# Performance work log

Hardware: AMD Instinct MI355X
Metric: run time of the kernel (lower is better)

The kernel has to match this reference:

```python
import jax, jax.numpy as jnp
import numpy as np

WS = 7            # cubic window
HEADS = 6
DIM = 96          # attention channel dim (concat of two half-streams)
CH = 48           # per-stream channels (dim // 2)
HID = 384         # int(dim * mlp_ratio)
N = WS ** 3       # 343 tokens per window
EPS = 1e-5


def _rel_pos_index():
    c = np.stack(np.meshgrid(np.arange(WS), np.arange(WS), np.arange(WS), indexing='ij')).reshape(3, -1)
    rel = (c[:, :, None] - c[:, None, :]).transpose(1, 2, 0) + (WS - 1)
    rel[:, :, 0] *= (2 * WS - 1) * (2 * WS - 1)
    rel[:, :, 1] *= (2 * WS - 1)
    return rel.sum(-1)  # (N, N) int

RPI = jnp.asarray(_rel_pos_index())


def _ln(x, g, b):
    m = x.mean(-1, keepdims=True)
    v = ((x - m) ** 2).mean(-1, keepdims=True)
    return (x - m) * jax.lax.rsqrt(v + EPS) * g + b


def _win_part(x):
    B, H, W, T, C = x.shape
    x = x.reshape(B, H // WS, WS, W // WS, WS, T // WS, WS, C)
    return x.transpose(0, 1, 3, 5, 2, 4, 6, 7).reshape(-1, WS, WS, WS, C)


def _win_rev(w, B, H, W, T):
    C = w.shape[-1]
    x = w.reshape(B, H // WS, W // WS, T // WS, WS, WS, WS, C)
    return x.transpose(0, 1, 4, 2, 5, 3, 6, 7).reshape(B, H, W, T, C)


def _chessboard(wa, wb, gd, gh, gw):
    C = wa.shape[-1]
    a = wa.reshape(gd, gh, gw, WS, WS, WS, C)
    b = wb.reshape(gd, gh, gw, WS, WS, WS, C)
    i = jnp.arange(gd)[:, None, None]
    j = jnp.arange(gh)[None, :, None]
    k = jnp.arange(gw)[None, None, :]
    m = (((i + j + k) % 2) == 0)[..., None, None, None, None]
    return (jnp.where(m, a, b).reshape(-1, WS, WS, WS, C),
            jnp.where(m, b, a).reshape(-1, WS, WS, WS, C))


def _attn(x, mask, rpb, qkv_w, qkv_b, proj_w, proj_b):
    B_, n, C = x.shape
    hd = C // HEADS
    qkv = (x @ qkv_w + qkv_b).reshape(B_, n, 3, HEADS, hd).transpose(2, 0, 3, 1, 4)
    q, k, v = qkv[0] * (hd ** -0.5), qkv[1], qkv[2]
    att = jnp.einsum('bhnd,bhmd->bhnm', q, k)
    att = att + rpb[RPI].transpose(2, 0, 1)[None]   # relative position bias gather
    att = att + mask[:, None]                        # shift mask; B_ == nW since B == 1
    att = jax.nn.softmax(att, axis=-1)
    out = jnp.einsum('bhnm,bhmd->bhnd', att, v).transpose(0, 2, 1, 3).reshape(B_, n, C)
    return out @ proj_w + proj_b


def _mlp(x, w1, b1, w2, b2):
    return jax.nn.gelu(x @ w1 + b1, approximate=False) @ w2 + b2


def _forward(x_a, x_b, mask_matrix, n1a_g, n1a_b, n1b_g, n1b_b,
             rpb_a, qkvw_a, qkvb_a, projw_a, projb_a,
             rpb_b, qkvw_b, qkvb_b, projw_b, projb_b,
             n2a_g, n2a_b, n2b_g, n2b_b,
             fc1w_a, fc1b_a, fc2w_a, fc2b_a, fc1w_b, fc1b_b, fc2w_b, fc2b_b,
             gw1, gw2, gb2, H, W, T):
    B, L, _ = x_a.shape
    sa0, sb0 = x_a, x_b
    a = _ln(x_a, n1a_g, n1a_b).reshape(B, H, W, T, CH)
    b = _ln(x_b, n1b_g, n1b_b).reshape(B, H, W, T, CH)
    # chessboard cross-stream shuffle of windows (shifted-window branch)
    ca, cb = _chessboard(_win_part(a), _win_part(b), H // WS, W // WS, T // WS)
    a_cr = _win_rev(ca, B, H, W, T)
    b_cr = _win_rev(cb, B, H, W, T)
    neg, pos, dims = (-3, -3, -3), (3, 3, 3), (1, 2, 3)
    sa, sb = jnp.roll(a, neg, dims), jnp.roll(b, neg, dims)
    sac, sbc = jnp.roll(a_cr, neg, dims), jnp.roll(b_cr, neg, dims)
    xa_w = _win_part(jnp.concatenate([sa, sbc], -1)).reshape(-1, N, DIM)
    xb_w = _win_part(jnp.concatenate([sb, sac], -1)).reshape(-1, N, DIM)
    oa = _attn(xa_w, mask_matrix, rpb_a, qkvw_a, qkvb_a, projw_a, projb_a)
    ob = _attn(xb_w, mask_matrix, rpb_b, qkvw_b, qkvb_b, projw_b, projb_b)
    oa = jnp.roll(_win_rev(oa.reshape(-1, WS, WS, WS, DIM), B, H, W, T), pos, dims)[..., :CH].reshape(B, L, CH)
    ob = jnp.roll(_win_rev(ob.reshape(-1, WS, WS, WS, DIM), B, H, W, T), pos, dims)[..., :CH].reshape(B, L, CH)
    x_a = sa0 + oa
    x_b = sb0 + ob
    x_a = x_a + _mlp(_ln(x_a, n2a_g, n2a_b), fc1w_a, fc1b_a, fc2w_a, fc2b_a)
    x_b = x_b + _mlp(_ln(x_b, n2b_g, n2b_b), fc1w_b, fc1b_b, fc2w_b, fc2b_b)
    g = jax.nn.sigmoid(jnp.maximum(x_a.mean(1) @ gw1, 0.0) @ gw2 + gb2)[:, :, None]  # (B,1,1)
    x_a = x_a + g * x_b
    return x_a, x_b


def setup_inputs():
    key = jax.random.key(0)
    ks = iter(jax.random.split(key, 24))
    H = W = T = 35
    L = H * W * T
    nW = (H // WS) * (W // WS) * (T // WS)
    p = lambda shape: jax.random.normal(next(ks), shape, jnp.float32) * 0.02
    d = {
        'x_a': jax.random.normal(next(ks), (1, L, CH), jnp.float32),
        'x_b': jax.random.normal(next(ks), (1, L, CH), jnp.float32),
        'mask_matrix': jax.random.normal(next(ks), (nW, N, N), jnp.float32),
        'n1a_g': jnp.ones((CH,), jnp.float32), 'n1a_b': jnp.zeros((CH,), jnp.float32),
        'n1b_g': jnp.ones((CH,), jnp.float32), 'n1b_b': jnp.zeros((CH,), jnp.float32),
        'rpb_a': p(((2 * WS - 1) ** 3, HEADS)),
        'qkvw_a': p((DIM, 3 * DIM)), 'qkvb_a': jnp.zeros((3 * DIM,), jnp.float32),
        'projw_a': p((DIM, DIM)), 'projb_a': jnp.zeros((DIM,), jnp.float32),
        'rpb_b': p(((2 * WS - 1) ** 3, HEADS)),
        'qkvw_b': p((DIM, 3 * DIM)), 'qkvb_b': jnp.zeros((3 * DIM,), jnp.float32),
        'projw_b': p((DIM, DIM)), 'projb_b': jnp.zeros((DIM,), jnp.float32),
        'n2a_g': jnp.ones((CH,), jnp.float32), 'n2a_b': jnp.zeros((CH,), jnp.float32),
        'n2b_g': jnp.ones((CH,), jnp.float32), 'n2b_b': jnp.zeros((CH,), jnp.float32),
        'fc1w_a': p((CH, HID)), 'fc1b_a': jnp.zeros((HID,), jnp.float32),
        'fc2w_a': p((HID, CH)), 'fc2b_a': jnp.zeros((CH,), jnp.float32),
        'fc1w_b': p((CH, HID)), 'fc1b_b': jnp.zeros((HID,), jnp.float32),
        'fc2w_b': p((HID, CH)), 'fc2b_b': jnp.zeros((CH,), jnp.float32),
        'gw1': p((CH, CH // 4)), 'gw2': p((CH // 4, 1)),
        'gb2': jnp.full((1,), -2.0, jnp.float32),
        'H': H, 'W': W, 'T': T,
    }
    return d


def reference(x_a, x_b, mask_matrix, n1a_g, n1a_b, n1b_g, n1b_b,
              rpb_a, qkvw_a, qkvb_a, projw_a, projb_a,
              rpb_b, qkvw_b, qkvb_b, projw_b, projb_b,
              n2a_g, n2a_b, n2b_g, n2b_b,
              fc1w_a, fc1b_a, fc2w_a, fc2b_a, fc1w_b, fc1b_b, fc2w_b, fc2b_b,
              gw1, gw2, gb2, H, W, T):
    return _forward(x_a, x_b, mask_matrix, n1a_g, n1a_b, n1b_g, n1b_b,
                    rpb_a, qkvw_a, qkvb_a, projw_a, projb_a,
                    rpb_b, qkvw_b, qkvb_b, projw_b, projb_b,
                    n2a_g, n2a_b, n2b_g, n2b_b,
                    fc1w_a, fc1b_a, fc2w_a, fc2b_a, fc1w_b, fc1b_b, fc2w_b, fc2b_b,
                    gw1, gw2, gb2, H, W, T)
```

## Files before the change

kernel.cpp:

```cpp
#include <hip/hip_runtime.h>
#include <hip/hip_fp16.h>

#define LQ    42875
#define NTOK  343
#define X1SZ  2058000

#define OFF_MEAN 0
#define OFF_QKV  36928
#define OFF_WF   12500000
#define OFF_RPB  12600000
#define OFF_MASKH 13400000
#define MASKH_ELEMS 14706125ull
#define QKV_BYTES_NEEDED 56100000ull
#define MASKH_BYTES_NEEDED 83100000ull

typedef _Float16 f16x8 __attribute__((ext_vector_type(8)));
typedef float f32x4 __attribute__((ext_vector_type(4)));
union B128 { uint4 u; f16x8 h; _Float16 e[8]; };

__device__ __forceinline__ int src_index(int w, int i, int& par) {
  int gi = w / 25, gj = (w / 5) % 5, gk = w % 5;
  int ph = i / 49, pw = (i / 7) % 7, pt = i % 7;
  int hs = gi * 7 + ph + 3; if (hs >= 35) hs -= 35;
  int wd = gj * 7 + pw + 3; if (wd >= 35) wd -= 35;
  int td = gk * 7 + pt + 3; if (td >= 35) td -= 35;
  par = ((hs / 7) + (wd / 7) + (td / 7)) & 1;
  return (hs * 35 + wd) * 35 + td;
}

__global__ __launch_bounds__(64) void k_init(float* __restrict__ ws) {
  if (threadIdx.x < 49) ws[threadIdx.x] = 0.f;
}

__global__ __launch_bounds__(256) void k_pack(
    const float* __restrict__ w1a, const float* __restrict__ w1b,
    const float* __restrict__ w2a, const float* __restrict__ w2b,
    const float* __restrict__ qwa, const float* __restrict__ qwb,
    float* __restrict__ ws) {
  int idx = blockIdx.x * 256 + threadIdx.x;
  if (idx >= 17664) return;
  uint4* WFB = (uint4*)(ws + OFF_WF);
  unsigned short h[8];
  uint4* dst;
  if (idx < 10752) {
    int s = idx / 5376, r = idx - s * 5376;
    uint4* WF = WFB + (size_t)s * 5376;
    if (r < 3072) {
      int jn = r / 128, t = r - jn * 128, kk = t / 64, lane = t - kk * 64;
      int q = lane >> 4, n = lane & 15;
      const float* w1 = s ? w1b : w1a;
      int j = jn * 16 + n;
#pragma unroll
      for (int e = 0; e < 8; e++) {
        int k = kk * 32 + q * 8 + e;
        float v = (k < 48) ? w1[k * 384 + j] : 0.f;
        h[e] = __half_as_ushort(__float2half(v));
      }
    } else {
      int rr = r - 3072;
      int kt = rr / 192, t = rr - kt * 192, cn = t / 64, lane = t - cn * 64;
      int q = lane >> 4, n = lane & 15;
      const float* w2 = s ? w2b : w2a;
      int c = cn * 16 + n;
#pragma unroll
      for (int e = 0; e < 8; e++) {
        int j = kt * 32 + q * 8 + e;
        h[e] = __half_as_ushort(__float2half(w2[j * 48 + c]));
      }
    }
    dst = WF + r;
  } else {
    int idx2 = idx - 10752;
    int s = idx2 / 3456, r = idx2 - s * 3456;
    int jn = r / 192, t = r - jn * 192, kk = t / 64, lane = t - kk * 64;
    int q = lane >> 4, n = lane & 15;
    const float* qw = s ? qwb : qwa;
    int j = jn * 16 + n;
#pragma unroll
    for (int e = 0; e < 8; e++) {
      int k = kk * 32 + q * 8 + e;
      h[e] = __half_as_ushort(__float2half(qw[k * 288 + j]));
    }
    dst = WFB + 10752 + (size_t)s * 3456 + r;
  }
  uint4 u;
  u.x = (unsigned)h[0] | ((unsigned)h[1] << 16);
  u.y = (unsigned)h[2] | ((unsigned)h[3] << 16);
  u.z = (unsigned)h[4] | ((unsigned)h[5] << 16);
  u.w = (unsigned)h[6] | ((unsigned)h[7] << 16);
  *dst = u;
}

__global__ __launch_bounds__(256) void k_rpb(
    const float* __restrict__ rpa, const float* __restrict__ rpbp,
    float* __restrict__ ws) {
  int sh = blockIdx.y;
  int s = sh / 6, h = sh - s * 6;
  int idx = blockIdx.x * 256 + threadIdx.x;
  if (idx >= 117649) return;
  int ir = idx / 343, j = idx - ir * 343;
  int bi = (ir / 49) * 169 + ((ir / 7) % 7) * 13 + (ir % 7) + 1098;
  int bj = (j / 49) * 169 + ((j / 7) % 7) * 13 + (j % 7);
  const float* rp = s ? rpbp : rpa;
  ((__half*)(ws + OFF_RPB))[(size_t)sh * 117649 + idx] =
      __float2half(rp[(bi - bj) * 6 + h]);
}

__global__ __launch_bounds__(256) void k_maskh(
    const float* __restrict__ mask, __half* __restrict__ mh) {
  size_t i = ((size_t)blockIdx.x * 256 + threadIdx.x) * 4;
  if (i + 4 <= MASKH_ELEMS) {
    float4 v = *(const float4*)(mask + i);
    __half2* d = (__half2*)(mh + i);
    d[0] = __floats2half2_rn(v.x, v.y);
    d[1] = __floats2half2_rn(v.z, v.w);
  } else {
    for (; i < MASKH_ELEMS; i++) mh[i] = __float2half(mask[i]);
  }
}

__global__ __launch_bounds__(256) void k_qkv(
    const float* __restrict__ xa, const float* __restrict__ xb,
    const float* __restrict__ ga, const float* __restrict__ ba,
    const float* __restrict__ gb, const float* __restrict__ bb,
    const float* __restrict__ qba, const float* __restrict__ qbb,
    const float* __restrict__ ws, __half* __restrict__ qkvh) {
  __shared__ uint4 LDSB[2368];
  int s = blockIdx.z;
  int tid = threadIdx.x;
  int wid = tid >> 6, lane = tid & 63;
  int quad = lane >> 4, n15 = lane & 15;
  uint4* WR = LDSB + wid * 592;
  _Float16* th = (_Float16*)WR;
  int tbase = blockIdx.x * 64 + wid * 16;

  if (lane < 32) {
    int tt = lane & 15, which = lane >> 4;
    int t = tbase + tt;
    float v[48];
    bool wr = false, dup = false;
    if (t < LQ) {
      int w = t / 343, i = t - w * 343;
      int par; int src = src_index(w, i, par);
      const float* xr; const float* G; const float* B;
      bool doit;
      if (which == 0) { xr = (s ? xb : xa) + src * 48; G = s ? gb : ga; B = s ? bb : ba; doit = true; dup = (par == 1); }
      else            { xr = (s ? xa : xb) + src * 48; G = s ? ga : gb; B = s ? ba : bb; doit = (par == 0); }
      if (doit) {
        float sm = 0.f, sq = 0.f;
#pragma unroll
        for (int q4 = 0; q4 < 12; q4++) {
          float4 tv = ((const float4*)xr)[q4];
          v[4 * q4] = tv.x; v[4 * q4 + 1] = tv.y; v[4 * q4 + 2] = tv.z; v[4 * q4 + 3] = tv.w;
          sm += tv.x + tv.y + tv.z + tv.w;
          sq += tv.x * tv.x + tv.y * tv.y + tv.z * tv.z + tv.w * tv.w;
        }
        float m = sm * (1.f / 48.f);
        float r = rsqrtf(sq * (1.f / 48.f) - m * m + 1e-5f);
#pragma unroll
        for (int k = 0; k < 48; k++) v[k] = (v[k] - m) * r * G[k] + B[k];
        wr = true;
      }
    } else if (which == 0) {
#pragma unroll
      for (int k = 0; k < 48; k++) v[k] = 0.f;
      wr = true; dup = true;
    }
    if (wr) {
#pragma unroll
      for (int c6 = 0; c6 < 6; c6++) {
        unsigned short h[8];
#pragma unroll
        for (int e = 0; e < 8; e++) h[e] = __half_as_ushort(__float2half(v[c6 * 8 + e]));
        uint4 u;
        u.x = (unsigned)h[0] | ((unsigned)h[1] << 16);
        u.y = (unsigned)h[2] | ((unsigned)h[3] << 16);
        u.z = (unsigned)h[4] | ((unsigned)h[5] << 16);
        u.w = (unsigned)h[6] | ((unsigned)h[7] << 16);
        WR[(which * 6 + c6) * 16 + tt] = u;
        if (dup) WR[(6 + c6) * 16 + tt] = u;
      }
    }
  }

  B128 ax0, ax1, ax2;
  ax0.u = WR[(0 + quad) * 16 + n15];
  ax1.u = WR[(4 + quad) * 16 + n15];
  ax2.u = WR[(8 + quad) * 16 + n15];

  const uint4* QF = (const uint4*)(ws + OFF_WF) + 10752 + (size_t)s * 3456;
  const float* QB = s ? qbb : qba;
  const f32x4 ZC = {0.f, 0.f, 0.f, 0.f};

  for (int jn = 0; jn < 18; jn++) {
    B128 b0, b1, b2;
    b0.u = QF[(jn * 3 + 0) * 64 + lane];
    b1.u = QF[(jn * 3 + 1) * 64 + lane];
    b2.u = QF[(jn * 3 + 2) * 64 + lane];
    f32x4 c = __builtin_amdgcn_mfma_f32_16x16x32_f16(ax0.h, b0.h, ZC, 0, 0, 0);
    c = __builtin_amdgcn_mfma_f32_16x16x32_f16(ax1.h, b1.h, c, 0, 0, 0);
    c = __builtin_amdgcn_mfma_f32_16x16x32_f16(ax2.h, b2.h, c, 0, 0, 0);
    float bias = QB[jn * 16 + n15];
    float scale = (jn < 6) ? 0.25f : 1.0f;
#pragma unroll
    for (int r = 0; r < 4; r++)
      th[(quad * 4 + r) * 296 + jn * 16 + n15] = (_Float16)((c[r] + bias) * scale);
  }
  for (int e = lane; e < 576; e += 64) {
    int row = e / 36, cc = e - row * 36;
    int t = tbase + row;
    if (t < LQ)
      ((uint4*)qkvh)[(size_t)(s * LQ + t) * 36 + cc] = WR[row * 37 + cc];
  }
}

template <typename MT>
__global__ __launch_bounds__(256) void k_attn(
    const __half* __restrict__ rpbmat,
    const MT* __restrict__ mask, __half* __restrict__ qkvh) {
  int bid = blockIdx.x;
  int xcd = bid & 7, q8 = bid >> 3;
  int u = q8 / 12, inst = q8 - u * 12;
  int w = u * 8 + xcd;
  if (w >= 125) return;
  int s = inst & 1, h = inst >> 1;

  __shared__ uint4 FRAG[1664];
  uint4* Kf4 = FRAG;
  uint4* Vf4 = FRAG + 704;
  uint4* Pb4 = FRAG + 1408;
  _Float16* Vfh = (_Float16*)(FRAG + 704);
  _Float16* Pbh = (_Float16*)(FRAG + 1408);

  int tid = threadIdx.x;
  const uint4 Z4 = {0u, 0u, 0u, 0u};
  for (int e = tid; e < 1408; e += 256) FRAG[e] = Z4;
  __syncthreads();

  size_t wbase = (size_t)((s * 125 + w) * NTOK) * 288;
  for (int i = tid; i < NTOK; i += 256) {
    const uint4* row = (const uint4*)(qkvh + wbase + (size_t)i * 288) + (h * 2);
    uint4 k0 = row[12], k1 = row[13];
    B128 v0, v1; v0.u = row[24]; v1.u = row[25];
    int n = i & 15, it = i >> 4;
    Kf4[it * 32 + n] = k0;
    Kf4[it * 32 + 16 + n] = k1;
    int vbase = ((i >> 5) * 64 + ((i >> 3) & 3) * 16) * 8 + (i & 7);
#pragma unroll
    for (int d = 0; d < 8; d++) {
      Vfh[vbase + d * 8] = v0.e[d];
      Vfh[vbase + (d + 8) * 8] = v1.e[d];
    }
  }
  __syncthreads();

  int wid = tid >> 6, lane = tid & 63;
  int quad = lane >> 4, n15 = lane & 15;
  int jj = n15 & 7, hi = n15 >> 3;
  const f32x4 ZC = {0.f, 0.f, 0.f, 0.f};
  __half* obh = qkvh;
  const __half* rbase = rpbmat + (size_t)(s * 6 + h) * 117649;

  int pA[4], pB[4];
#pragma unroll
  for (int r = 0; r < 4; r++) {
    int ra = hi * 16 + quad * 4 + r;
    int rb = (2 + hi) * 16 + quad * 4 + r;
    ra ^= (ra >> 3) & 7;
    rb ^= (rb >> 3) & 7;
    pA[r] = wid * 512 + ra * 8 + jj;
    pB[r] = wid * 512 + rb * 8 + jj;
  }
  int rdrow = wid * 64 + (lane ^ ((lane >> 3) & 7));

  for (int it = wid; it < 22; it += 4) {
    int i0 = it * 16;
    const MT* mr[4]; const __half* rr[4];
#pragma unroll
    for (int r = 0; r < 4; r++) {
      int ir = i0 + quad * 4 + r; if (ir > 342) ir = 342;
      mr[r] = mask + (size_t)(w * NTOK + ir) * NTOK;
      rr[r] = rbase + ir * NTOK;
    }
    B128 qbits;
    int qtok = i0 + n15;
    if (quad < 2 && qtok < NTOK)
      qbits.u = *((const uint4*)(qkvh + wbase + (size_t)qtok * 288) + h * 2 + (quad & 1));
    else
      qbits.u = Z4;
    f32x4 acc = ZC;
    float ls[4] = {0.f, 0.f, 0.f, 0.f};

    float mcur[8], mnxt[8], rcur[8], rnxt[8];
    {
      int ja = n15, jb = n15 + 16;
#pragma unroll
      for (int r = 0; r < 4; r++) {
        mcur[r] = (float)mr[r][ja]; mcur[4 + r] = (float)mr[r][jb];
        rcur[r] = (float)rr[r][ja]; rcur[4 + r] = (float)rr[r][jb];
      }
    }
    for (int j32 = 0; j32 < 11; j32++) {
      if (j32 < 10) {
        int ja = (j32 + 1) * 32 + n15, jb = ja + 16;
        bool vb = jb < NTOK;
#pragma unroll
        for (int r = 0; r < 4; r++) {
          mnxt[r] = (float)mr[r][ja];
          mnxt[4 + r] = vb ? (float)mr[r][jb] : -1e30f;
          rnxt[r] = (float)rr[r][ja];
          rnxt[4 + r] = vb ? (float)rr[r][jb] : 0.f;
        }
      }
      B128 kb0, kb1;
      kb0.u = Kf4[(j32 * 2) * 32 + ((quad & 1) << 4) + n15];
      kb1.u = Kf4[(j32 * 2 + 1) * 32 + ((quad & 1) << 4) + n15];
      if (quad >= 2) { kb0.u = Z4; kb1.u = Z4; }
      f32x4 s0 = __builtin_amdgcn_mfma_f32_16x16x32_f16(qbits.h, kb0.h, ZC, 0, 0, 0);
      f32x4 s1 = __builtin_amdgcn_mfma_f32_16x16x32_f16(qbits.h, kb1.h, ZC, 0, 0, 0);
      float p0[4], p1[4];
#pragma unroll
      for (int r = 0; r < 4; r++) {
        p0[r] = __expf(s0[r] + mcur[r] + rcur[r]);
        p1[r] = __expf(s1[r] + mcur[4 + r] + rcur[4 + r]);
        ls[r] += p0[r] + p1[r];
      }
#pragma unroll
      for (int r = 0; r < 4; r++) {
        Pbh[pA[r]] = (_Float16)p0[r];
        Pbh[pB[r]] = (_Float16)p1[r];
      }
      B128 pb, vbits;
      pb.u = Pb4[rdrow];
      vbits.u = Vf4[j32 * 64 + lane];
      acc = __builtin_amdgcn_mfma_f32_16x16x32_f16(pb.h, vbits.h, acc, 0, 0, 0);
#pragma unroll
      for (int e = 0; e < 8; e++) { mcur[e] = mnxt[e]; rcur[e] = rnxt[e]; }
    }
#pragma unroll
    for (int r = 0; r < 4; r++) {
      float v = ls[r];
      v += __shfl_xor(v, 1); v += __shfl_xor(v, 2);
      v += __shfl_xor(v, 4); v += __shfl_xor(v, 8);
      int ir = i0 + quad * 4 + r;
      if (ir < 343)
        obh[wbase + (size_t)ir * 288 + h * 16 + n15] = __float2half(acc[r] * (1.f / v));
    }
  }
}

__global__ __launch_bounds__(384) void k_proj(
    const __half* __restrict__ qkvh,
    const float* __restrict__ xa0, const float* __restrict__ xb0,
    const float* __restrict__ pwa, const float* __restrict__ pba,
    const float* __restrict__ pwb, const float* __restrict__ pbb,
    float* __restrict__ out) {
  int sw = blockIdx.x; int s = sw / 125, w = sw - s * 125;
  int i = threadIdx.x;
  if (i >= NTOK) return;
  const float* Wt = s ? pwb : pwa;
  const float* Bi = s ? pbb : pba;
  const uint4* orow = (const uint4*)(qkvh + (size_t)((s * 125 + w) * NTOK + i) * 288);
  float acc[48];
#pragma unroll
  for (int c = 0; c < 48; c++) acc[c] = 0.f;
#pragma unroll
  for (int k8 = 0; k8 < 12; k8++) {
    B128 ov; ov.u = orow[k8];
#pragma unroll
    for (int e = 0; e < 8; e++) {
      float x = (float)ov.e[e];
      const float* wr = Wt + (k8 * 8 + e) * 96;
#pragma unroll
      for (int c = 0; c < 48; c++) acc[c] = fmaf(x, wr[c], acc[c]);
    }
  }
  int par; int src = src_index(w, i, par);
  const float* x0 = (s ? xb0 : xa0) + src * 48;
  float* dst = out + s * X1SZ + src * 48;
#pragma unroll
  for (int q = 0; q < 12; q++) {
    float4 xv = ((const float4*)x0)[q];
    float4 o;
    o.x = xv.x + acc[4 * q + 0] + Bi[4 * q + 0];
    o.y = xv.y + acc[4 * q + 1] + Bi[4 * q + 1];
    o.z = xv.z + acc[4 * q + 2] + Bi[4 * q + 2];
    o.w = xv.w + acc[4 * q + 3] + Bi[4 * q + 3];
    ((float4*)dst)[q] = o;
  }
}

__global__ __launch_bounds__(256) void k_mlp(
    const float* __restrict__ g2a, const float* __restrict__ b2a,
    const float* __restrict__ g2b, const float* __restrict__ b2b,
    const float* __restrict__ fb1a, const float* __restrict__ fb2a,
    const float* __restrict__ fb1b, const float* __restrict__ fb2b,
    float* __restrict__ out, float* __restrict__ ws) {
  __shared__ uint4 Xf[512];
  __shared__ uint4 tbu[320];
  __shared__ float red[48];
  int s = blockIdx.z;
  int tid = threadIdx.x;
  int wid = tid >> 6, lane = tid & 63;
  int quad = lane >> 4, n15 = lane & 15;
  if (tid < 48) red[tid] = 0.f;
  __syncthreads();

  const float* B1 = s ? fb1b : fb1a;
  const float* B2 = s ? fb2b : fb2a;
  const uint4* W1F = (const uint4*)(ws + OFF_WF) + (size_t)s * 5376;
  const uint4* W2F = W1F + 3072;
  int tbase = blockIdx.x * 64 + wid * 16;
  float* outs = out + (size_t)s * X1SZ;

  if (lane < 16) {
    int t = tbase + lane;
    float v[48];
    if (t < LQ) {
      const float* row = outs + (size_t)t * 48;
      float sm = 0.f, sq = 0.f;
#pragma unroll
      for (int q4 = 0; q4 < 12; q4++) {
        float4 tv = ((const float4*)row)[q4];
        v[4 * q4] = tv.x; v[4 * q4 + 1] = tv.y; v[4 * q4 + 2] = tv.z; v[4 * q4 + 3] = tv.w;
        sm += tv.x + tv.y + tv.z + tv.w;
        sq += tv.x * tv.x + tv.y * tv.y + tv.z * tv.z + tv.w * tv.w;
      }
      float m = sm * (1.f / 48.f);
      float r = rsqrtf(sq * (1.f / 48.f) - m * m + 1e-5f);
      const float* G = s ? g2b : g2a;
      const float* B = s ? b2b : b2a;
#pragma unroll
      for (int k = 0; k < 48; k++) v[k] = (v[k] - m) * r * G[k] + B[k];
    } else {
#pragma unroll
      for (int k = 0; k < 48; k++) v[k] = 0.f;
    }
#pragma unroll
    for (int kc = 0; kc < 8; kc++) {
      uint4 u = {0u, 0u, 0u, 0u};
      if (kc < 6) {
        unsigned short h[8];
#pragma unroll
        for (int e = 0; e < 8; e++) h[e] = __half_as_ushort(__float2half(v[kc * 8 + e]));
        u.x = (unsigned)h[0] | ((unsigned)h[1] << 16);
        u.y = (unsigned)h[2] | ((unsigned)h[3] << 16);
        u.z = (unsigned)h[4] | ((unsigned)h[5] << 16);
        u.w = (unsigned)h[6] | ((unsigned)h[7] << 16);
      }
      Xf[wid * 128 + kc * 16 + lane] = u;
    }
  }

  _Float16* mytb = (_Float16*)(tbu + wid * 80);
  const uint4* mytb4 = tbu + wid * 80;
  const f32x4 ZC = {0.f, 0.f, 0.f, 0.f};
  f32x4 oacc[3] = {ZC, ZC, ZC};
  B128 ax0, ax1;
  ax0.u = Xf[wid * 128 + quad * 16 + n15];
  ax1.u = Xf[wid * 128 + (4 + quad) * 16 + n15];

  for (int kt = 0; kt < 12; kt++) {
    int jn0 = kt * 2, jn1 = jn0 + 1;
    B128 w0, w1, w2, w3;
    w0.u = W1F[jn0 * 128 + lane];
    w1.u = W1F[jn0 * 128 + 64 + lane];
    w2.u = W1F[jn1 * 128 + lane];
    w3.u = W1F[jn1 * 128 + 64 + lane];
    f32x4 a0 = __builtin_amdgcn_mfma_f32_16x16x32_f16(ax0.h, w0.h, ZC, 0, 0, 0);
    a0 = __builtin_amdgcn_mfma_f32_16x16x32_f16(ax1.h, w1.h, a0, 0, 0, 0);
    f32x4 a1 = __builtin_amdgcn_mfma_f32_16x16x32_f16(ax0.h, w2.h, ZC, 0, 0, 0);
    a1 = __builtin_amdgcn_mfma_f32_16x16x32_f16(ax1.h, w3.h, a1, 0, 0, 0);
    float bz0 = B1[jn0 * 16 + n15], bz1 = B1[jn1 * 16 + n15];
#pragma unroll
    for (int r = 0; r < 4; r++) {
      float h0 = a0[r] + bz0;
      h0 = 0.5f * h0 * (1.f + erff(h0 * 0.70710678118654752f));
      float h1 = a1[r] + bz1;
      h1 = 0.5f * h1 * (1.f + erff(h1 * 0.70710678118654752f));
      int rowb = (quad * 4 + r) * 40;
      mytb[rowb + n15] = (_Float16)h0;
      mytb[rowb + 16 + n15] = (_Float16)h1;
    }
    B128 pa; pa.u = mytb4[n15 * 5 + quad];
    B128 c0, c1, c2;
    c0.u = W2F[kt * 192 + lane];
    c1.u = W2F[kt * 192 + 64 + lane];
    c2.u = W2F[kt * 192 + 128 + lane];
    oacc[0] = __builtin_amdgcn_mfma_f32_16x16x32_f16(pa.h, c0.h, oacc[0], 0, 0, 0);
    oacc[1] = __builtin_amdgcn_mfma_f32_16x16x32_f16(pa.h, c1.h, oacc[1], 0, 0, 0);
    oacc[2] = __builtin_amdgcn_mfma_f32_16x16x32_f16(pa.h, c2.h, oacc[2], 0, 0, 0);
  }

  float b2v[3];
#pragma unroll
  for (int cn = 0; cn < 3; cn++) b2v[cn] = B2[cn * 16 + n15];
  float gsum[3] = {0.f, 0.f, 0.f};
#pragma unroll
  for (int r = 0; r < 4; r++) {
    int t = tbase + quad * 4 + r;
    bool val = t < LQ;
    float* orow = outs + (size_t)(val ? t : 0) * 48;
#pragma unroll
    for (int cn = 0; cn < 3; cn++) {
      float fin = 0.f;
      if (val) {
        fin = orow[cn * 16 + n15] + oacc[cn][r] + b2v[cn];
        orow[cn * 16 + n15] = fin;
      }
      gsum[cn] += fin;
    }
  }
  if (s == 0) {
#pragma unroll
    for (int cn = 0; cn < 3; cn++) {
      float v = gsum[cn];
      v += __shfl_xor(v, 16); v += __shfl_xor(v, 32);
      if (quad == 0) atomicAdd(&red[cn * 16 + n15], v);
    }
  }
  __syncthreads();
  if (s == 0 && tid < 48) atomicAdd(ws + OFF_MEAN + tid, red[tid]);
}

__global__ __launch_bounds__(64) void k_gate(
    const float* __restrict__ ws_mean, const float* __restrict__ gw1,
    const float* __restrict__ gw2, const float* __restrict__ gb2,
    float* __restrict__ g) {
  int j = threadIdx.x;
  float t = 0.f;
  if (j < 12) {
    for (int c = 0; c < 48; c++)
      t = fmaf(ws_mean[c] * (1.f / (float)LQ), gw1[c * 12 + j], t);
    t = fmaxf(t, 0.f) * gw2[j];
  }
  for (int off = 32; off > 0; off >>= 1) t += __shfl_down(t, off);
  if (j == 0) *g = 1.f / (1.f + __expf(-(t + gb2[0])));
}

__global__ __launch_bounds__(256) void k_gadd(float* __restrict__ out,
                                              const float* __restrict__ g) {
  int i = blockIdx.x * 256 + threadIdx.x;
  if (i >= X1SZ / 4) return;
  float gv = *g;
  float4* a = (float4*)out;
  const float4* b = (const float4*)(out + X1SZ);
  float4 x = a[i], y = b[i];
  x.x = fmaf(gv, y.x, x.x);
  x.y = fmaf(gv, y.y, x.y);
  x.z = fmaf(gv, y.z, x.z);
  x.w = fmaf(gv, y.w, x.w);
  a[i] = x;
}

extern "C" void kernel_launch(void* const* d_in, const int* in_sizes, int n_in,
                              void* d_out, int out_size, void* d_ws, size_t ws_size,
                              hipStream_t stream) {
  const float* xa    = (const float*)d_in[0];
  const float* xb    = (const float*)d_in[1];
  const float* mask  = (const float*)d_in[2];
  const float* n1ag  = (const float*)d_in[3];
  const float* n1ab  = (const float*)d_in[4];
  const float* n1bg  = (const float*)d_in[5];
  const float* n1bb  = (const float*)d_in[6];
  const float* rpba  = (const float*)d_in[7];
  const float* qkvwa = (const float*)d_in[8];
  const float* qkvba = (const float*)d_in[9];
  const float* pwa   = (const float*)d_in[10];
  const float* pba   = (const float*)d_in[11];
  const float* rpbb  = (const float*)d_in[12];
  const float* qkvwb = (const float*)d_in[13];
  const float* qkvbb = (const float*)d_in[14];
  const float* pwb   = (const float*)d_in[15];
  const float* pbb   = (const float*)d_in[16];
  const float* n2ag  = (const float*)d_in[17];
  const float* n2ab  = (const float*)d_in[18];
  const float* n2bg  = (const float*)d_in[19];
  const float* n2bb  = (const float*)d_in[20];
  const float* w1a   = (const float*)d_in[21];
  const float* fb1a  = (const float*)d_in[22];
  const float* w2a   = (const float*)d_in[23];
  const float* fb2a  = (const float*)d_in[24];
  const float* w1b   = (const float*)d_in[25];
  const float* fb1b  = (const float*)d_in[26];
  const float* w2b   = (const float*)d_in[27];
  const float* fb2b  = (const float*)d_in[28];
  const float* gw1   = (const float*)d_in[29];
  const float* gw2   = (const float*)d_in[30];
  const float* gb2   = (const float*)d_in[31];
  float* ws  = (float*)d_ws;
  float* out = (float*)d_out;

  if (ws_size < QKV_BYTES_NEEDED) return;
  __half* qkvh = (__half*)(ws + OFF_QKV);
  bool bigmask = ws_size >= MASKH_BYTES_NEEDED;

  hipLaunchKernelGGL(k_init, dim3(1), dim3(64), 0, stream, ws);
  hipLaunchKernelGGL(k_pack, dim3(69), dim3(256), 0, stream,
                     w1a, w1b, w2a, w2b, qkvwa, qkvwb, ws);
  hipLaunchKernelGGL(k_rpb, dim3(460, 12), dim3(256), 0, stream,
                     rpba, rpbb, ws);
  if (bigmask)
    hipLaunchKernelGGL(k_maskh, dim3(14362), dim3(256), 0, stream,
                       mask, (__half*)(ws + OFF_MASKH));
  hipLaunchKernelGGL(k_qkv, dim3(670, 1, 2), dim3(256), 0, stream,
                     xa, xb, n1ag, n1ab, n1bg, n1bb,
                     qkvba, qkvbb, ws, qkvh);
  if (bigmask)
    hipLaunchKernelGGL((k_attn<__half>), dim3(1536), dim3(256), 0, stream,
                       (const __half*)(ws + OFF_RPB),
                       (const __half*)(ws + OFF_MASKH), qkvh);
  else
    hipLaunchKernelGGL((k_attn<float>), dim3(1536), dim3(256), 0, stream,
                       (const __half*)(ws + OFF_RPB), mask, qkvh);
  hipLaunchKernelGGL(k_proj, dim3(250), dim3(384), 0, stream,
                     qkvh, xa, xb, pwa, pba, pwb, pbb, out);
  hipLaunchKernelGGL(k_mlp, dim3(670, 1, 2), dim3(256), 0, stream,
                     n2ag, n2ab, n2bg, n2bb,
                     fb1a, fb2a, fb1b, fb2b, out, ws);
  hipLaunchKernelGGL(k_gate, dim3(1), dim3(64), 0, stream,
                     ws + OFF_MEAN, gw1, gw2, gb2, ws + OFF_MEAN + 48);
  hipLaunchKernelGGL(k_gadd, dim3(2011), dim3(256), 0, stream,
                     out, ws + OFF_MEAN + 48);
}
```

Before: 438.2 us.

## Transpose QK^T MFMA and pad mask/bias rows for vectorized bias loads

Swaps the QK^T MFMA operands so each lane holds one query row and four consecutive key columns. This lets the mask and relative-position-bias rows be read as 8-byte vector loads and pre-summed in half2. Mask and bias matrices are repacked with rows padded to 344 halves for alignment, and the P staging writes become packed uint2 stores with a new swizzle. The row-sum reduction is simplified to two cross-quad shuffles. The risks are fp16 summation of mask plus bias, and a mask-conversion kernel that now launches one block per row with poorer coalescing.

```diff
diff --git a/kernel.cpp b/kernel.cpp
--- a/kernel.cpp
+++ b/kernel.cpp
@@ -10,13 +10,13 @@
 #define OFF_WF   12500000
 #define OFF_RPB  12600000
 #define OFF_MASKH 13400000
-#define MASKH_ELEMS 14706125ull
 #define QKV_BYTES_NEEDED 56100000ull
 #define MASKH_BYTES_NEEDED 83100000ull
 
 typedef _Float16 f16x8 __attribute__((ext_vector_type(8)));
 typedef float f32x4 __attribute__((ext_vector_type(4)));
 union B128 { uint4 u; f16x8 h; _Float16 e[8]; };
+union U2H { unsigned u; __half2 h; };
 
 __device__ __forceinline__ int src_index(int w, int i, int& par) {
   int gi = w / 25, gj = (w / 5) % 5, gk = w % 5;
@@ -102,21 +102,18 @@
   int bi = (ir / 49) * 169 + ((ir / 7) % 7) * 13 + (ir % 7) + 1098;
   int bj = (j / 49) * 169 + ((j / 7) % 7) * 13 + (j % 7);
   const float* rp = s ? rpbp : rpa;
-  ((__half*)(ws + OFF_RPB))[(size_t)sh * 117649 + idx] =
+  ((__half*)(ws + OFF_RPB))[(size_t)sh * 117992 + ir * 344 + j] =
       __float2half(rp[(bi - bj) * 6 + h]);
 }
 
 __global__ __launch_bounds__(256) void k_maskh(
     const float* __restrict__ mask, __half* __restrict__ mh) {
-  size_t i = ((size_t)blockIdx.x * 256 + threadIdx.x) * 4;
-  if (i + 4 <= MASKH_ELEMS) {
-    float4 v = *(const float4*)(mask + i);
-    __half2* d = (__half2*)(mh + i);
-    d[0] = __floats2half2_rn(v.x, v.y);
-    d[1] = __floats2half2_rn(v.z, v.w);
-  } else {
-    for (; i < MASKH_ELEMS; i++) mh[i] = __float2half(mask[i]);
-  }
+  int row = blockIdx.x;
+  const float* src = mask + (size_t)row * 343;
+  __half* dst = mh + (size_t)row * 344;
+  for (int c = threadIdx.x; c < 343; c += 256)
+    dst[c] = __float2half(src[c]);
+  if (threadIdx.x == 0) dst[343] = __float2half(0.f);
 }
 
 __global__ __launch_bounds__(256) void k_qkv(
@@ -214,10 +211,10 @@
   }
 }
 
-template <typename MT>
+template <bool H16>
 __global__ __launch_bounds__(256) void k_attn(
     const __half* __restrict__ rpbmat,
-    const MT* __restrict__ mask, __half* __restrict__ qkvh) {
+    const void* __restrict__ maskp, __half* __restrict__ qkvh) {
   int bid = blockIdx.x;
   int xcd = bid & 7, q8 = bid >> 3;
   int u = q8 / 12, inst = q8 - u * 12;
@@ -228,7 +225,6 @@
   __shared__ uint4 FRAG[1664];
   uint4* Kf4 = FRAG;
   uint4* Vf4 = FRAG + 704;
-  uint4* Pb4 = FRAG + 1408;
   _Float16* Vfh = (_Float16*)(FRAG + 704);
   _Float16* Pbh = (_Float16*)(FRAG + 1408);
 
@@ -256,32 +252,24 @@
 
   int wid = tid >> 6, lane = tid & 63;
   int quad = lane >> 4, n15 = lane & 15;
-  int jj = n15 & 7, hi = n15 >> 3;
   const f32x4 ZC = {0.f, 0.f, 0.f, 0.f};
   __half* obh = qkvh;
-  const __half* rbase = rpbmat + (size_t)(s * 6 + h) * 117649;
-
-  int pA[4], pB[4];
-#pragma unroll
-  for (int r = 0; r < 4; r++) {
-    int ra = hi * 16 + quad * 4 + r;
-    int rb = (2 + hi) * 16 + quad * 4 + r;
-    ra ^= (ra >> 3) & 7;
-    rb ^= (rb >> 3) & 7;
-    pA[r] = wid * 512 + ra * 8 + jj;
-    pB[r] = wid * 512 + rb * 8 + jj;
-  }
-  int rdrow = wid * 64 + (lane ^ ((lane >> 3) & 7));
+  const __half* rbase = rpbmat + (size_t)(s * 6 + h) * 117992;
+
+  _Float16* Pw = Pbh + wid * 512;
+  int slotA = quad ^ (n15 & 6);
+  int slotB = (4 + quad) ^ (n15 & 6);
+  int rslot = (2 * quad) ^ (n15 & 6);
+  int ja0 = quad * 4;
 
   for (int it = wid; it < 22; it += 4) {
     int i0 = it * 16;
-    const MT* mr[4]; const __half* rr[4];
-#pragma unroll
-    for (int r = 0; r < 4; r++) {
-      int ir = i0 + quad * 4 + r; if (ir > 342) ir = 342;
-      mr[r] = mask + (size_t)(w * NTOK + ir) * NTOK;
-      rr[r] = rbase + ir * NTOK;
-    }
+    int irow = i0 + n15; if (irow > 342) irow = 342;
+    const __half* rrow = rbase + (size_t)irow * 344;
+    const __half* mrow = nullptr; const float* mrowf = nullptr;
+    if constexpr (H16) mrow = (const __half*)maskp + ((size_t)w * 343 + irow) * 344;
+    else mrowf = (const float*)maskp + ((size_t)w * 343 + irow) * 343;
+
     B128 qbits;
     int qtok = i0 + n15;
     if (quad < 2 && qtok < NTOK)
@@ -289,62 +277,79 @@
     else
       qbits.u = Z4;
     f32x4 acc = ZC;
-    float ls[4] = {0.f, 0.f, 0.f, 0.f};
-
-    float mcur[8], mnxt[8], rcur[8], rnxt[8];
-    {
-      int ja = n15, jb = n15 + 16;
-#pragma unroll
-      for (int r = 0; r < 4; r++) {
-        mcur[r] = (float)mr[r][ja]; mcur[4 + r] = (float)mr[r][jb];
-        rcur[r] = (float)rr[r][ja]; rcur[4 + r] = (float)rr[r][jb];
-      }
-    }
+    float ls = 0.f;
+
+    float bcur[8], bnxt[8];
+    auto loadb = [&](int jt, float* b) {
+      if constexpr (H16) {
+        const __half* mp = mrow + jt * 32 + ja0;
+        const __half* rp2 = rrow + jt * 32 + ja0;
+        uint2 ma = *(const uint2*)mp;
+        uint2 mb = *(const uint2*)(mp + 16);
+        uint2 ra = *(const uint2*)rp2;
+        uint2 rb = *(const uint2*)(rp2 + 16);
+        U2H x0, x1, x2, x3, y0, y1, y2, y3;
+        x0.u = ma.x; x1.u = ma.y; x2.u = mb.x; x3.u = mb.y;
+        y0.u = ra.x; y1.u = ra.y; y2.u = rb.x; y3.u = rb.y;
+        float2 f;
+        f = __half22float2(__hadd2(x0.h, y0.h)); b[0] = f.x; b[1] = f.y;
+        f = __half22float2(__hadd2(x1.h, y1.h)); b[2] = f.x; b[3] = f.y;
+        f = __half22float2(__hadd2(x2.h, y2.h)); b[4] = f.x; b[5] = f.y;
+        f = __half22float2(__hadd2(x3.h, y3.h)); b[6] = f.x; b[7] = f.y;
+      } else {
+        const float* mp = mrowf + jt * 32 + ja0;
+        const __half* rp2 = rrow + jt * 32 + ja0;
+#pragma unroll
+        for (int r = 0; r < 4; r++) {
+          b[r] = mp[r] + __half2float(rp2[r]);
+          b[4 + r] = mp[16 + r] + __half2float(rp2[16 + r]);
+        }
+      }
+    };
+    loadb(0, bcur);
+
     for (int j32 = 0; j32 < 11; j32++) {
-      if (j32 < 10) {
-        int ja = (j32 + 1) * 32 + n15, jb = ja + 16;
-        bool vb = jb < NTOK;
-#pragma unroll
-        for (int r = 0; r < 4; r++) {
-          mnxt[r] = (float)mr[r][ja];
-          mnxt[4 + r] = vb ? (float)mr[r][jb] : -1e30f;
-          rnxt[r] = (float)rr[r][ja];
-          rnxt[4 + r] = vb ? (float)rr[r][jb] : 0.f;
-        }
-      }
+      if (j32 < 10) loadb(j32 + 1, bnxt);
       B128 kb0, kb1;
       kb0.u = Kf4[(j32 * 2) * 32 + ((quad & 1) << 4) + n15];
       kb1.u = Kf4[(j32 * 2 + 1) * 32 + ((quad & 1) << 4) + n15];
       if (quad >= 2) { kb0.u = Z4; kb1.u = Z4; }
-      f32x4 s0 = __builtin_amdgcn_mfma_f32_16x16x32_f16(qbits.h, kb0.h, ZC, 0, 0, 0);
-      f32x4 s1 = __builtin_amdgcn_mfma_f32_16x16x32_f16(qbits.h, kb1.h, ZC, 0, 0, 0);
+      f32x4 s0 = __builtin_amdgcn_mfma_f32_16x16x32_f16(kb0.h, qbits.h, ZC, 0, 0, 0);
+      f32x4 s1 = __builtin_amdgcn_mfma_f32_16x16x32_f16(kb1.h, qbits.h, ZC, 0, 0, 0);
+      bool last = (j32 == 10);
       float p0[4], p1[4];
 #pragma unroll
       for (int r = 0; r < 4; r++) {
-        p0[r] = __expf(s0[r] + mcur[r] + rcur[r]);
-        p1[r] = __expf(s1[r] + mcur[4 + r] + rcur[4 + r]);
-        ls[r] += p0[r] + p1[r];
-      }
-#pragma unroll
-      for (int r = 0; r < 4; r++) {
-        Pbh[pA[r]] = (_Float16)p0[r];
-        Pbh[pB[r]] = (_Float16)p1[r];
-      }
-      B128 pb, vbits;
-      pb.u = Pb4[rdrow];
+        float b1 = bcur[4 + r];
+        if (last && (quad * 4 + r) >= 7) b1 = -1e30f;
+        p0[r] = __expf(s0[r] + bcur[r]);
+        p1[r] = __expf(s1[r] + b1);
+        ls += p0[r] + p1[r];
+      }
+      U2H c0, c1, c2, c3;
+      c0.h = __floats2half2_rn(p0[0], p0[1]);
+      c1.h = __floats2half2_rn(p0[2], p0[3]);
+      c2.h = __floats2half2_rn(p1[0], p1[1]);
+      c3.h = __floats2half2_rn(p1[2], p1[3]);
+      uint2 w0; w0.x = c0.u; w0.y = c1.u;
+      uint2 w1; w1.x = c2.u; w1.y = c3.u;
+      *(uint2*)(Pw + n15 * 32 + slotA * 4) = w0;
+      *(uint2*)(Pw + n15 * 32 + slotB * 4) = w1;
+      B128 pa, vbits;
+      pa.u = *(const uint4*)(Pw + n15 * 32 + rslot * 4);
       vbits.u = Vf4[j32 * 64 + lane];
-      acc = __builtin_amdgcn_mfma_f32_16x16x32_f16(pb.h, vbits.h, acc, 0, 0, 0);
-#pragma unroll
-      for (int e = 0; e < 8; e++) { mcur[e] = mnxt[e]; rcur[e] = rnxt[e]; }
-    }
+      acc = __builtin_amdgcn_mfma_f32_16x16x32_f16(pa.h, vbits.h, acc, 0, 0, 0);
+#pragma unroll
+      for (int e = 0; e < 8; e++) bcur[e] = bnxt[e];
+    }
+    ls += __shfl_xor(ls, 16);
+    ls += __shfl_xor(ls, 32);
 #pragma unroll
     for (int r = 0; r < 4; r++) {
-      float v = ls[r];
-      v += __shfl_xor(v, 1); v += __shfl_xor(v, 2);
-      v += __shfl_xor(v, 4); v += __shfl_xor(v, 8);
+      float lr = __shfl(ls, quad * 4 + r);
       int ir = i0 + quad * 4 + r;
       if (ir < 343)
-        obh[wbase + (size_t)ir * 288 + h * 16 + n15] = __float2half(acc[r] * (1.f / v));
+        obh[wbase + (size_t)ir * 288 + h * 16 + n15] = __float2half(acc[r] * (1.f / lr));
     }
   }
 }
@@ -601,18 +606,18 @@
   hipLaunchKernelGGL(k_rpb, dim3(460, 12), dim3(256), 0, stream,
                      rpba, rpbb, ws);
   if (bigmask)
-    hipLaunchKernelGGL(k_maskh, dim3(14362), dim3(256), 0, stream,
+    hipLaunchKernelGGL(k_maskh, dim3(42875), dim3(256), 0, stream,
                        mask, (__half*)(ws + OFF_MASKH));
   hipLaunchKernelGGL(k_qkv, dim3(670, 1, 2), dim3(256), 0, stream,
                      xa, xb, n1ag, n1ab, n1bg, n1bb,
                      qkvba, qkvbb, ws, qkvh);
   if (bigmask)
-    hipLaunchKernelGGL((k_attn<__half>), dim3(1536), dim3(256), 0, stream,
+    hipLaunchKernelGGL((k_attn<true>), dim3(1536), dim3(256), 0, stream,
                        (const __half*)(ws + OFF_RPB),
-                       (const __half*)(ws + OFF_MASKH), qkvh);
+                       (const void*)(ws + OFF_MASKH), qkvh);
   else
-    hipLaunchKernelGGL((k_attn<float>), dim3(1536), dim3(256), 0, stream,
-                       (const __half*)(ws + OFF_RPB), mask, qkvh);
+    hipLaunchKernelGGL((k_attn<false>), dim3(1536), dim3(256), 0, stream,
+                       (const __half*)(ws + OFF_RPB), (const void*)mask, qkvh);
   hipLaunchKernelGGL(k_proj, dim3(250), dim3(384), 0, stream,
                      qkvh, xa, xb, pwa, pba, pwb, pbb, out);
   hipLaunchKernelGGL(k_mlp, dim3(670, 1, 2), dim3(256), 0, stream,
```

New measurement: 449.1 us. 2.5% more time.
